# Performance work log

Hardware: AMD Instinct MI355X
Metric: run time of the kernel (lower is better)

The kernel has to match this reference:

```python
import jax, jax.numpy as jnp
import numpy as np

MARGIN = 0.5          # triplet_margin
CLS_W = 1.0           # classification_weight
TRI_W = 1.0           # triplet_weight
SMOOTH = 0.1          # CrossEntropyLoss label_smoothing
PD_EPS = 1e-6         # torch pairwise_distance eps inside TripletMarginLoss


def setup_inputs() -> dict:
    key = jax.random.key(0)
    k1, k2, k3 = jax.random.split(key, 3)
    B, D, C = 8192, 128, 1000
    logits = jax.random.normal(k1, (B, C), dtype=jnp.float32)
    emb = jax.random.normal(k2, (B, D), dtype=jnp.float32)
    emb = emb / jnp.linalg.norm(emb, axis=1, keepdims=True)  # L2-normalized per docstring
    labels = jax.random.randint(k3, (B,), 0, C, dtype=jnp.int32)
    return {"logits": logits, "embeddings": emb, "labels": labels}


def _combined_loss(logits, embeddings, labels):
    # --- cross entropy with label smoothing 0.1 ---
    logp = jax.nn.log_softmax(logits, axis=-1)
    nll = -jnp.take_along_axis(logp, labels[:, None], axis=-1)[:, 0]
    smooth_term = -logp.mean(axis=-1)  # eps/C * sum(-logp) == eps * mean(-logp)
    cls_loss = ((1.0 - SMOOTH) * nll + SMOOTH * smooth_term).mean()

    # --- batch-hard triplet mining (vectorized over all rows) ---
    B = embeddings.shape[0]
    sq = jnp.sum(embeddings * embeddings, axis=1)
    # squared pairwise distances [B,B]; monotone in true distance, so ranking matches cdist
    d2 = sq[:, None] + sq[None, :] - 2.0 * (embeddings @ embeddings.T)
    eq = labels[:, None] == labels[None, :]
    pos_mask = eq & ~jnp.eye(B, dtype=bool)   # same class, not self
    neg_mask = ~eq
    big = jnp.finfo(d2.dtype).max
    hardest_pos = jnp.argmax(jnp.where(pos_mask, d2, -big), axis=1)  # farthest positive
    hardest_neg = jnp.argmin(jnp.where(neg_mask, d2, big), axis=1)   # closest negative
    valid = pos_mask.any(axis=1) & neg_mask.any(axis=1)

    # --- TripletMarginLoss(margin, p=2) over valid triplets ---
    a = embeddings
    p = embeddings[hardest_pos]
    n = embeddings[hardest_neg]
    d_ap = jnp.linalg.norm(a - p + PD_EPS, axis=1)  # torch adds eps inside the norm
    d_an = jnp.linalg.norm(a - n + PD_EPS, axis=1)
    per_row = jnp.maximum(d_ap - d_an + MARGIN, 0.0)
    cnt = jnp.sum(valid)
    triplet_loss = jnp.where(
        cnt > 0,
        jnp.sum(jnp.where(valid, per_row, 0.0)) / jnp.maximum(cnt, 1).astype(per_row.dtype),
        jnp.zeros((), per_row.dtype),
    )

    return CLS_W * cls_loss + TRI_W * triplet_loss


def reference(logits, embeddings, labels):
    return _combined_loss(logits, embeddings, labels)
```

## Files before the change

### kernel.cpp

```cpp
#include <hip/hip_runtime.h>

#define NB 8192
#define ND 128
#define NC 1000
#define NCH 64
#define CHS 128
#define NPAIR (NCH * (NCH + 1) / 2)
#define CAP 64
#define NRB (NB / 4)

typedef __attribute__((ext_vector_type(8))) short bf16x8;
typedef __attribute__((ext_vector_type(4))) float f32x4;

__device__ __forceinline__ unsigned short f2bf(float f) {
    unsigned int u = __float_as_uint(f);
    return (unsigned short)((u + 0x7fffu + ((u >> 16) & 1u)) >> 16);
}

__global__ __launch_bounds__(256) void ce_prep_kernel(const float* __restrict__ logits,
                                                      const float* __restrict__ emb,
                                                      const int* __restrict__ labels,
                                                      unsigned short* __restrict__ ebf,
                                                      float* __restrict__ cls_part,
                                                      int* __restrict__ cnt) {
    int wave = threadIdx.x >> 6, lane = threadIdx.x & 63;
    int r = blockIdx.x * 4 + wave;

    if (blockIdx.x == 0) {
        for (int k = threadIdx.x; k < NC; k += 256) cnt[k] = 0;
    }

    {
        const float* erow = emb + (size_t)r * ND;
        float2 v = *(const float2*)(erow + lane * 2);
        unsigned int packed = (unsigned int)f2bf(v.x) | ((unsigned int)f2bf(v.y) << 16);
        *(unsigned int*)(ebf + (size_t)r * ND + lane * 2) = packed;
    }

    const float* x = logits + (size_t)r * NC;
    float4 q0 = *(const float4*)(x + 4 * lane);
    float4 q1 = *(const float4*)(x + 256 + 4 * lane);
    float4 q2 = *(const float4*)(x + 512 + 4 * lane);
    float4 q3;
    bool a3 = (192 + lane) < 250;
    if (a3) q3 = *(const float4*)(x + 768 + 4 * lane);
    else q3 = make_float4(-3.4e38f, -3.4e38f, -3.4e38f, -3.4e38f);

    float m = fmaxf(fmaxf(fmaxf(q0.x, q0.y), fmaxf(q0.z, q0.w)),
                    fmaxf(fmaxf(q1.x, q1.y), fmaxf(q1.z, q1.w)));
    m = fmaxf(m, fmaxf(fmaxf(q2.x, q2.y), fmaxf(q2.z, q2.w)));
    m = fmaxf(m, fmaxf(fmaxf(q3.x, q3.y), fmaxf(q3.z, q3.w)));
    float s = (q0.x + q0.y + q0.z + q0.w) + (q1.x + q1.y + q1.z + q1.w) +
              (q2.x + q2.y + q2.z + q2.w) +
              (a3 ? (q3.x + q3.y + q3.z + q3.w) : 0.f);
#pragma unroll
    for (int o = 32; o >= 1; o >>= 1) {
        m = fmaxf(m, __shfl_xor(m, o));
        s += __shfl_xor(s, o);
    }
    float se = expf(q0.x - m) + expf(q0.y - m) + expf(q0.z - m) + expf(q0.w - m) +
               expf(q1.x - m) + expf(q1.y - m) + expf(q1.z - m) + expf(q1.w - m) +
               expf(q2.x - m) + expf(q2.y - m) + expf(q2.z - m) + expf(q2.w - m) +
               expf(q3.x - m) + expf(q3.y - m) + expf(q3.z - m) + expf(q3.w - m);
#pragma unroll
    for (int o = 32; o >= 1; o >>= 1) se += __shfl_xor(se, o);
    float xl = x[labels[r]];
    float v = (m + logf(se)) - 0.9f * xl - 0.1f * (s * (1.0f / NC));
    if (lane == 0) cls_part[r] = v;
}

__global__ __launch_bounds__(256) void bucket_kernel(const int* __restrict__ labels,
                                                     int* __restrict__ cnt,
                                                     int* __restrict__ lists) {
    int r = blockIdx.x * 256 + threadIdx.x;
    int c = labels[r];
    int slot = atomicAdd(&cnt[c], 1);
    if (slot < CAP) lists[c * CAP + slot] = r;
}

__global__ __launch_bounds__(256, 4) void mine_kernel(const unsigned short* __restrict__ ebf,
                                                      const int* __restrict__ labels,
                                                      float* __restrict__ part) {
    __shared__ unsigned short btile[CHS * ND];
    __shared__ float colbuf[4][CHS];
    int tid = threadIdx.x;
    int wave = tid >> 6, lane = tid & 63;
    int col = lane & 15, grp = lane >> 4;

    int t = blockIdx.x, a = 0;
    while (t >= NCH - a) { t -= NCH - a; ++a; }
    int b = a + t;

    int ibase = a * CHS + wave * 32;
    int jbase = b * CHS;

#pragma unroll
    for (int rep = 0; rep < 8; ++rep) {
        int row = (tid >> 4) + rep * 16;
        const unsigned short* src =
            ebf + (size_t)(jbase + row) * ND + (((tid & 15) ^ (row & 7)) << 3);
        unsigned short* dst = btile + (size_t)((tid >> 6) * 4 + rep * 16) * ND;
        __builtin_amdgcn_global_load_lds(
            (const __attribute__((address_space(1))) unsigned int*)src,
            (__attribute__((address_space(3))) unsigned int*)dst, 16, 0, 0);
    }

    bf16x8 af[2][4];
#pragma unroll
    for (int ic = 0; ic < 2; ++ic) {
        const unsigned short* ap = ebf + (size_t)(ibase + ic * 16 + col) * ND + (grp << 3);
#pragma unroll
        for (int kc = 0; kc < 4; ++kc) af[ic][kc] = *(const bf16x8*)(ap + kc * 32);
    }
    int li[8];
#pragma unroll
    for (int ic = 0; ic < 2; ++ic)
#pragma unroll
        for (int r = 0; r < 4; ++r) li[ic * 4 + r] = labels[ibase + ic * 16 + grp * 4 + r];
    int ljall[8];
#pragma unroll
    for (int st = 0; st < 8; ++st) ljall[st] = labels[jbase + st * 16 + col];

    float bn[8];
    float colmax[8];
#pragma unroll
    for (int k = 0; k < 8; ++k) { bn[k] = -3.4e38f; colmax[k] = -3.4e38f; }

    __syncthreads();

#pragma unroll
    for (int st = 0; st < 8; ++st) {
        bf16x8 bfr[4];
#pragma unroll
        for (int kc = 0; kc < 4; ++kc) {
            int chunk = (grp + 4 * kc) ^ (col & 7);
            bfr[kc] = *(const bf16x8*)(btile + (size_t)(st * 16 + col) * ND + chunk * 8);
        }
        f32x4 acc[2] = {{0.f, 0.f, 0.f, 0.f}, {0.f, 0.f, 0.f, 0.f}};
#pragma unroll
        for (int kc = 0; kc < 4; ++kc)
#pragma unroll
            for (int ic = 0; ic < 2; ++ic)
                acc[ic] = __builtin_amdgcn_mfma_f32_16x16x32_bf16(af[ic][kc], bfr[kc],
                                                                  acc[ic], 0, 0, 0);
        int lj = ljall[st];
        float cm = -3.4e38f;
#pragma unroll
        for (int ic = 0; ic < 2; ++ic)
#pragma unroll
            for (int r = 0; r < 4; ++r) {
                float mv = (lj == li[ic * 4 + r]) ? -3.4e38f : acc[ic][r];
                bn[ic * 4 + r] = fmaxf(bn[ic * 4 + r], mv);
                cm = fmaxf(cm, mv);
            }
        cm = fmaxf(cm, __shfl_xor(cm, 16));
        cm = fmaxf(cm, __shfl_xor(cm, 32));
        colmax[st] = cm;
    }

#pragma unroll
    for (int k = 0; k < 8; ++k)
#pragma unroll
        for (int msk = 1; msk <= 8; msk <<= 1)
            bn[k] = fmaxf(bn[k], __shfl_xor(bn[k], msk));
    if (col == 0) {
#pragma unroll
        for (int ic = 0; ic < 2; ++ic)
#pragma unroll
            for (int r = 0; r < 4; ++r) {
                int gi = ibase + ic * 16 + grp * 4 + r;
                part[(size_t)gi * NCH + b] = bn[ic * 4 + r];
            }
    }

    if (a != b) {
        if (lane < 16) {
#pragma unroll
            for (int st = 0; st < 8; ++st) colbuf[wave][st * 16 + lane] = colmax[st];
        }
        __syncthreads();
        if (tid < CHS) {
            float m = fmaxf(fmaxf(colbuf[0][tid], colbuf[1][tid]),
                            fmaxf(colbuf[2][tid], colbuf[3][tid]));
            part[(size_t)(jbase + tid) * NCH + a] = m;
        }
    }
}

__global__ __launch_bounds__(256) void reduce_kernel(const float* __restrict__ e,
                                                     const int* __restrict__ labels,
                                                     const float* __restrict__ part,
                                                     const int* __restrict__ cnt,
                                                     const int* __restrict__ lists,
                                                     const float* __restrict__ cls_part,
                                                     float4* __restrict__ blk) {
    __shared__ float sp[4], sv[4], sc[4];
    int wave = threadIdx.x >> 6, lane = threadIdx.x & 63;
    int r = blockIdx.x * 4 + wave;
    int g = lane >> 3, sl = lane & 7;

    float nb = part[(size_t)r * NCH + lane];
#pragma unroll
    for (int o = 1; o <= 32; o <<= 1) nb = fmaxf(nb, __shfl_xor(nb, o));
    float d_an = sqrtf(fmaxf(2.0f - 2.0f * nb, 0.0f));

    int myl = labels[r];
    int ctot = cnt[myl];
    int n = min(ctot, CAP);
    const float* a = e + (size_t)r * ND;

    float4 a0 = *(const float4*)(a + sl * 16);
    float4 a1 = *(const float4*)(a + sl * 16 + 4);
    float4 a2 = *(const float4*)(a + sl * 16 + 8);
    float4 a3 = *(const float4*)(a + sl * 16 + 12);

    float best = -1.0f;
    int jp = r;
    for (int base = 0; base < n; base += 8) {
        int idx = base + g;
        bool ok = (idx < n);
        int j2 = ok ? lists[myl * CAP + idx] : r;
        const float* p = e + (size_t)j2 * ND;
        float4 p0 = *(const float4*)(p + sl * 16);
        float4 p1 = *(const float4*)(p + sl * 16 + 4);
        float4 p2 = *(const float4*)(p + sl * 16 + 8);
        float4 p3 = *(const float4*)(p + sl * 16 + 12);
        float d, ss = 0.f;
        d = a0.x - p0.x; ss += d * d; d = a0.y - p0.y; ss += d * d;
        d = a0.z - p0.z; ss += d * d; d = a0.w - p0.w; ss += d * d;
        d = a1.x - p1.x; ss += d * d; d = a1.y - p1.y; ss += d * d;
        d = a1.z - p1.z; ss += d * d; d = a1.w - p1.w; ss += d * d;
        d = a2.x - p2.x; ss += d * d; d = a2.y - p2.y; ss += d * d;
        d = a2.z - p2.z; ss += d * d; d = a2.w - p2.w; ss += d * d;
        d = a3.x - p3.x; ss += d * d; d = a3.y - p3.y; ss += d * d;
        d = a3.z - p3.z; ss += d * d; d = a3.w - p3.w; ss += d * d;
        ss += __shfl_xor(ss, 1);
        ss += __shfl_xor(ss, 2);
        ss += __shfl_xor(ss, 4);
        float d2v = (ok && j2 != r) ? ss : -2.0f;
        if (d2v > best || (d2v == best && j2 < jp)) { best = d2v; jp = j2; }
    }
#pragma unroll
    for (int msk = 8; msk <= 32; msk <<= 1) {
        float ob = __shfl_xor(best, msk);
        int oj = __shfl_xor(jp, msk);
        if (ob > best || (ob == best && oj < jp)) { best = ob; jp = oj; }
    }
    bool valid = (ctot >= 2) && (ctot < NB);

    const float* p = e + (size_t)jp * ND;
    float2 av = *(const float2*)(a + lane * 2);
    float2 pv = *(const float2*)(p + lane * 2);
    float dx = av.x - pv.x + 1e-6f, dy = av.y - pv.y + 1e-6f;
    float ss = dx * dx + dy * dy;
#pragma unroll
    for (int o = 32; o >= 1; o >>= 1) ss += __shfl_xor(ss, o);
    float d_ap = sqrtf(ss);

    if (lane == 0) {
        sp[wave] = valid ? fmaxf(d_ap - d_an + 0.5f, 0.0f) : 0.0f;
        sv[wave] = valid ? 1.0f : 0.0f;
        sc[wave] = cls_part[r];
    }
    __syncthreads();
    if (threadIdx.x == 0)
        blk[blockIdx.x] = make_float4(sp[0] + sp[1] + sp[2] + sp[3],
                                      sv[0] + sv[1] + sv[2] + sv[3],
                                      sc[0] + sc[1] + sc[2] + sc[3], 0.f);
}

__global__ __launch_bounds__(1024) void fin_kernel(const float4* __restrict__ blk,
                                                   float* __restrict__ out) {
    __shared__ float sc[16], sp[16], sn[16];
    int t = threadIdx.x;
    int wave = t >> 6, lane = t & 63;
    float tp = 0.f, tv = 0.f, c = 0.f;
    for (int k = t; k < NRB; k += 1024) {
        float4 q = blk[k];
        tp += q.x;
        tv += q.y;
        c += q.z;
    }
#pragma unroll
    for (int o = 32; o >= 1; o >>= 1) {
        tp += __shfl_xor(tp, o);
        tv += __shfl_xor(tv, o);
        c += __shfl_xor(c, o);
    }
    if (lane == 0) { sp[wave] = tp; sn[wave] = tv; sc[wave] = c; }
    __syncthreads();
    if (t == 0) {
        float P = 0.f, V = 0.f, C = 0.f;
        for (int w = 0; w < 16; ++w) { P += sp[w]; V += sn[w]; C += sc[w]; }
        float tri = V > 0.5f ? P / V : 0.0f;
        out[0] = C * (1.0f / NB) + tri;
    }
}

extern "C" void kernel_launch(void* const* d_in, const int* in_sizes, int n_in,
                              void* d_out, int out_size, void* d_ws, size_t ws_size,
                              hipStream_t stream) {
    const float* logits = (const float*)d_in[0];
    const float* emb = (const float*)d_in[1];
    const int* labels = (const int*)d_in[2];

    char* w = (char*)d_ws;
    unsigned short* ebf = (unsigned short*)w;
    float* part = (float*)(w + 2097152);
    float* cls_part = (float*)(w + 4194304);
    int* cnt = (int*)(w + 4227072);
    int* lists = (int*)(w + 4231168);
    float4* blk = (float4*)(w + 4493312);

    ce_prep_kernel<<<NB / 4, 256, 0, stream>>>(logits, emb, labels, ebf, cls_part, cnt);
    bucket_kernel<<<NB / 256, 256, 0, stream>>>(labels, cnt, lists);
    mine_kernel<<<NPAIR, 256, 0, stream>>>(ebf, labels, part);
    reduce_kernel<<<NRB, 256, 0, stream>>>(emb, labels, part, cnt, lists, cls_part, blk);
    fin_kernel<<<1, 1024, 0, stream>>>(blk, (float*)d_out);
}
```

Before: 49.74 us.

## Process multiple column chunks per mining block with double-buffered LDS staging

Each mining block now keeps its row tile's A fragments and labels in registers and loops over up to six column chunks. The next B tile is prefetched into a second LDS buffer while the current one is consumed. This cuts the block count from one per chunk pair to a few hundred, amortising the A-fragment and label loads and overlapping global-to-LDS copies with MFMA work. In exchange the LDS footprint doubles, occupancy bounds drop to two blocks per CU, and load balance is uneven because blocks handle between one and six chunks.

```diff
diff --git a/kernel.cpp b/kernel.cpp
--- a/kernel.cpp
+++ b/kernel.cpp
@@ -5,7 +5,8 @@
 #define NC 1000
 #define NCH 64
 #define CHS 128
-#define NPAIR (NCH * (NCH + 1) / 2)
+#define SL 6
+#define NBLK 374
 #define CAP 64
 #define NRB (NB / 4)
 
@@ -78,31 +79,41 @@
     if (slot < CAP) lists[c * CAP + slot] = r;
 }
 
-__global__ __launch_bounds__(256, 4) void mine_kernel(const unsigned short* __restrict__ ebf,
+__global__ __launch_bounds__(256, 2) void mine_kernel(const unsigned short* __restrict__ ebf,
                                                       const int* __restrict__ labels,
                                                       float* __restrict__ part) {
-    __shared__ unsigned short btile[CHS * ND];
-    __shared__ float colbuf[4][CHS];
+    __shared__ unsigned short btile[2][CHS * ND];
+    __shared__ float colbuf[2][4][CHS];
+    __shared__ int lj_lds[SL * CHS];
     int tid = threadIdx.x;
     int wave = tid >> 6, lane = tid & 63;
     int col = lane & 15, grp = lane >> 4;
 
-    int t = blockIdx.x, a = 0;
-    while (t >= NCH - a) { t -= NCH - a; ++a; }
-    int b = a + t;
-
+    int s = blockIdx.x, a = 0;
+    while (s >= (NCH - a + SL - 1) / SL) { s -= (NCH - a + SL - 1) / SL; ++a; }
+    int b0 = a + SL * s;
     int ibase = a * CHS + wave * 32;
-    int jbase = b * CHS;
-
-#pragma unroll
-    for (int rep = 0; rep < 8; ++rep) {
-        int row = (tid >> 4) + rep * 16;
-        const unsigned short* src =
-            ebf + (size_t)(jbase + row) * ND + (((tid & 15) ^ (row & 7)) << 3);
-        unsigned short* dst = btile + (size_t)((tid >> 6) * 4 + rep * 16) * ND;
-        __builtin_amdgcn_global_load_lds(
-            (const __attribute__((address_space(1))) unsigned int*)src,
-            (__attribute__((address_space(3))) unsigned int*)dst, 16, 0, 0);
+
+#define STAGE(buf, jb0)                                                              \
+    do {                                                                             \
+        _Pragma("unroll")                                                            \
+        for (int rep = 0; rep < 8; ++rep) {                                          \
+            int row = (tid >> 4) + rep * 16;                                         \
+            const unsigned short* src =                                              \
+                ebf + (size_t)((jb0) + row) * ND + (((tid & 15) ^ (row & 7)) << 3);  \
+            unsigned short* dst =                                                    \
+                &btile[buf][0] + (size_t)((tid >> 6) * 4 + rep * 16) * ND;           \
+            __builtin_amdgcn_global_load_lds(                                        \
+                (const __attribute__((address_space(1))) unsigned int*)src,          \
+                (__attribute__((address_space(3))) unsigned int*)dst, 16, 0, 0);     \
+        }                                                                            \
+    } while (0)
+
+    STAGE(0, b0 * CHS);
+
+    for (int k = tid; k < SL * CHS; k += 256) {
+        int idx = b0 * CHS + k;
+        lj_lds[k] = labels[min(idx, NB - 1)];
     }
 
     bf16x8 af[2][4];
@@ -117,74 +128,78 @@
     for (int ic = 0; ic < 2; ++ic)
 #pragma unroll
         for (int r = 0; r < 4; ++r) li[ic * 4 + r] = labels[ibase + ic * 16 + grp * 4 + r];
-    int ljall[8];
-#pragma unroll
-    for (int st = 0; st < 8; ++st) ljall[st] = labels[jbase + st * 16 + col];
-
-    float bn[8];
-    float colmax[8];
-#pragma unroll
-    for (int k = 0; k < 8; ++k) { bn[k] = -3.4e38f; colmax[k] = -3.4e38f; }
 
     __syncthreads();
 
-#pragma unroll
-    for (int st = 0; st < 8; ++st) {
-        bf16x8 bfr[4];
-#pragma unroll
-        for (int kc = 0; kc < 4; ++kc) {
-            int chunk = (grp + 4 * kc) ^ (col & 7);
-            bfr[kc] = *(const bf16x8*)(btile + (size_t)(st * 16 + col) * ND + chunk * 8);
+    for (int t = 0; t < SL; ++t) {
+        int b = b0 + t;
+        if (b >= NCH) break;
+        int cur = t & 1;
+        if (t + 1 < SL && b + 1 < NCH) STAGE(cur ^ 1, (b + 1) * CHS);
+
+        int jbase = b * CHS;
+        float bn[8], colmax[8];
+#pragma unroll
+        for (int k = 0; k < 8; ++k) { bn[k] = -3.4e38f; colmax[k] = -3.4e38f; }
+
+        const unsigned short* bt = &btile[cur][0];
+#pragma unroll
+        for (int st = 0; st < 8; ++st) {
+            bf16x8 bfr[4];
+#pragma unroll
+            for (int kc = 0; kc < 4; ++kc) {
+                int chunk = (grp + 4 * kc) ^ (col & 7);
+                bfr[kc] = *(const bf16x8*)(bt + (size_t)(st * 16 + col) * ND + chunk * 8);
+            }
+            f32x4 acc[2] = {{0.f, 0.f, 0.f, 0.f}, {0.f, 0.f, 0.f, 0.f}};
+#pragma unroll
+            for (int kc = 0; kc < 4; ++kc)
+#pragma unroll
+                for (int ic = 0; ic < 2; ++ic)
+                    acc[ic] = __builtin_amdgcn_mfma_f32_16x16x32_bf16(af[ic][kc], bfr[kc],
+                                                                      acc[ic], 0, 0, 0);
+            int lj = lj_lds[t * CHS + st * 16 + col];
+            float cm = -3.4e38f;
+#pragma unroll
+            for (int ic = 0; ic < 2; ++ic)
+#pragma unroll
+                for (int r = 0; r < 4; ++r) {
+                    float mv = (lj == li[ic * 4 + r]) ? -3.4e38f : acc[ic][r];
+                    bn[ic * 4 + r] = fmaxf(bn[ic * 4 + r], mv);
+                    cm = fmaxf(cm, mv);
+                }
+            cm = fmaxf(cm, __shfl_xor(cm, 16));
+            cm = fmaxf(cm, __shfl_xor(cm, 32));
+            colmax[st] = cm;
         }
-        f32x4 acc[2] = {{0.f, 0.f, 0.f, 0.f}, {0.f, 0.f, 0.f, 0.f}};
-#pragma unroll
-        for (int kc = 0; kc < 4; ++kc)
+
+#pragma unroll
+        for (int k = 0; k < 8; ++k)
+#pragma unroll
+            for (int msk = 1; msk <= 8; msk <<= 1)
+                bn[k] = fmaxf(bn[k], __shfl_xor(bn[k], msk));
+        if (col == 0) {
 #pragma unroll
             for (int ic = 0; ic < 2; ++ic)
-                acc[ic] = __builtin_amdgcn_mfma_f32_16x16x32_bf16(af[ic][kc], bfr[kc],
-                                                                  acc[ic], 0, 0, 0);
-        int lj = ljall[st];
-        float cm = -3.4e38f;
-#pragma unroll
-        for (int ic = 0; ic < 2; ++ic)
-#pragma unroll
-            for (int r = 0; r < 4; ++r) {
-                float mv = (lj == li[ic * 4 + r]) ? -3.4e38f : acc[ic][r];
-                bn[ic * 4 + r] = fmaxf(bn[ic * 4 + r], mv);
-                cm = fmaxf(cm, mv);
-            }
-        cm = fmaxf(cm, __shfl_xor(cm, 16));
-        cm = fmaxf(cm, __shfl_xor(cm, 32));
-        colmax[st] = cm;
-    }
-
-#pragma unroll
-    for (int k = 0; k < 8; ++k)
-#pragma unroll
-        for (int msk = 1; msk <= 8; msk <<= 1)
-            bn[k] = fmaxf(bn[k], __shfl_xor(bn[k], msk));
-    if (col == 0) {
-#pragma unroll
-        for (int ic = 0; ic < 2; ++ic)
-#pragma unroll
-            for (int r = 0; r < 4; ++r) {
-                int gi = ibase + ic * 16 + grp * 4 + r;
-                part[(size_t)gi * NCH + b] = bn[ic * 4 + r];
-            }
-    }
-
-    if (a != b) {
+#pragma unroll
+                for (int r = 0; r < 4; ++r) {
+                    int gi = ibase + ic * 16 + grp * 4 + r;
+                    part[(size_t)gi * NCH + b] = bn[ic * 4 + r];
+                }
+        }
+
         if (lane < 16) {
 #pragma unroll
-            for (int st = 0; st < 8; ++st) colbuf[wave][st * 16 + lane] = colmax[st];
+            for (int st = 0; st < 8; ++st) colbuf[cur][wave][st * 16 + lane] = colmax[st];
         }
         __syncthreads();
-        if (tid < CHS) {
-            float m = fmaxf(fmaxf(colbuf[0][tid], colbuf[1][tid]),
-                            fmaxf(colbuf[2][tid], colbuf[3][tid]));
+        if (b != a && tid < CHS) {
+            float m = fmaxf(fmaxf(colbuf[cur][0][tid], colbuf[cur][1][tid]),
+                            fmaxf(colbuf[cur][2][tid], colbuf[cur][3][tid]));
             part[(size_t)(jbase + tid) * NCH + a] = m;
         }
     }
+#undef STAGE
 }
 
 __global__ __launch_bounds__(256) void reduce_kernel(const float* __restrict__ e,
@@ -314,7 +329,7 @@
 
     ce_prep_kernel<<<NB / 4, 256, 0, stream>>>(logits, emb, labels, ebf, cls_part, cnt);
     bucket_kernel<<<NB / 256, 256, 0, stream>>>(labels, cnt, lists);
-    mine_kernel<<<NPAIR, 256, 0, stream>>>(ebf, labels, part);
+    mine_kernel<<<NBLK, 256, 0, stream>>>(ebf, labels, part);
     reduce_kernel<<<NRB, 256, 0, stream>>>(emb, labels, part, cnt, lists, cls_part, blk);
     fin_kernel<<<1, 1024, 0, stream>>>(blk, (float*)d_out);
 }
```

New measurement: 54.80 us. 10.2% more time.
